# Kernel tuning notes

Measured on AMD Instinct MI355X. Metric: run time of the kernel, lower is better.

Reference implementation:

```python
import jax, jax.numpy as jnp
import numpy as np

B, H, L, DK, DV = 4, 16, 1024, 64, 64

def setup_inputs() -> dict:
    key = jax.random.key(0)
    k1, k2, k3, k4 = jax.random.split(key, 4)
    Q = jax.random.normal(k1, (B, H, L, DK), dtype=jnp.float32)
    K = jax.random.normal(k2, (B, H, L, DK), dtype=jnp.float32)
    V = jax.random.normal(k3, (B, H, L, DV), dtype=jnp.float32)
    attn_mask = jax.random.randint(k4, (B, H, L, L), 0, 2).astype(jnp.bool_)
    return {"Q": Q, "K": K, "V": V, "attn_mask": attn_mask}

def reference(Q, K, V, attn_mask):
    # NOTE: original torch code uses d_k = Q.size(1) == n_heads (a bug kept for fidelity)
    scale = 1.0 / jnp.sqrt(jnp.asarray(Q.shape[1], dtype=Q.dtype))
    scores = jnp.einsum('bhqd,bhkd->bhqk', Q, K) * scale
    scores = jnp.where(attn_mask, jnp.asarray(-1e9, dtype=scores.dtype), scores)
    attn = jax.nn.softmax(scores, axis=-1)
    context = jnp.einsum('bhqk,bhkv->bhqv', attn, V)
    return (context, attn)
```

## Files before the change

kernel.cpp:

```cpp
#include <hip/hip_runtime.h>
#include <hip/hip_bf16.h>

typedef _Float16 half8 __attribute__((ext_vector_type(8)));
typedef _Float16 half4 __attribute__((ext_vector_type(4)));
typedef _Float16 half2v __attribute__((ext_vector_type(2)));
typedef __fp16 fp16x2 __attribute__((ext_vector_type(2)));
typedef float f32x4 __attribute__((ext_vector_type(4)));

#define BH_ 64
#define L_ 1024
#define DK_ 64

__device__ __forceinline__ unsigned short f2h(float f) {
    _Float16 h = (_Float16)f;
    return __builtin_bit_cast(unsigned short, h);
}
__device__ __forceinline__ unsigned int pk2h(float a, float b) {
    fp16x2 h = __builtin_amdgcn_cvt_pkrtz(a, b);
    return __builtin_bit_cast(unsigned int, h);
}

__global__ void prep_k(const float* __restrict__ K, unsigned short* __restrict__ Kh) {
    int idx = blockIdx.x * 256 + threadIdx.x;
    float4 v = reinterpret_cast<const float4*>(K)[idx];
    ushort4 o;
    o.x = f2h(v.x); o.y = f2h(v.y); o.z = f2h(v.z); o.w = f2h(v.w);
    reinterpret_cast<ushort4*>(Kh)[idx] = o;
}

__global__ void prep_v(const float* __restrict__ V, unsigned short* __restrict__ Vt) {
    __shared__ float lds[64][65];
    int bh = blockIdx.x >> 4, kt = blockIdx.x & 15;
    int t = threadIdx.x;
    const float* Vb = V + ((size_t)bh * L_ + kt * 64) * DK_;
#pragma unroll
    for (int it = 0; it < 4; ++it) {
        int idx = it * 256 + t;
        int row = idx >> 4, c4 = idx & 15;
        float4 v = reinterpret_cast<const float4*>(Vb + (size_t)row * DK_)[c4];
        lds[row][c4 * 4 + 0] = v.x; lds[row][c4 * 4 + 1] = v.y;
        lds[row][c4 * 4 + 2] = v.z; lds[row][c4 * 4 + 3] = v.w;
    }
    __syncthreads();
    unsigned short* Vtb = Vt + (size_t)bh * 64 * L_ + kt * 64;
#pragma unroll
    for (int it = 0; it < 4; ++it) {
        int idx = it * 256 + t;
        int n = idx >> 4, c4 = idx & 15;
        ushort4 o;
        o.x = f2h(lds[c4 * 4 + 0][n]);
        o.y = f2h(lds[c4 * 4 + 1][n]);
        o.z = f2h(lds[c4 * 4 + 2][n]);
        o.w = f2h(lds[c4 * 4 + 3][n]);
        *reinterpret_cast<ushort4*>(Vtb + (size_t)n * L_ + c4 * 4) = o;
    }
}

__global__ __launch_bounds__(256, 4) void attn_main(
    const float* __restrict__ Q, const int* __restrict__ mask,
    const unsigned short* __restrict__ Kh, const unsigned short* __restrict__ Vt,
    float* __restrict__ ctx_out, float* __restrict__ attn_out)
{
    const int qt = blockIdx.x, bh = blockIdx.y;
    const int tid = threadIdx.x;
    const int w = tid >> 6;
    const int lane = tid & 63;
    const int lg = lane >> 4, lr = lane & 15;
    const int q0 = qt * 16;

    __shared__ unsigned char mnib[16][272];
    __shared__ float red[2][4][16];
    __shared__ union {
        unsigned short p[16][1024];
        float ctxbuf[4][16][68];
    } u;

    auto paddr = [&](int row, int col) -> unsigned short* {
        unsigned byte = (unsigned)row * 2048u +
                        (((unsigned)col * 2u) ^ (((unsigned)(row & 7)) << 4));
        return (unsigned short*)((char*)&u.p[0][0] + byte);
    };

#pragma unroll
    for (int rr = 0; rr < 4; ++rr) {
        const int row = w * 4 + rr;
        const int* mrow = mask + ((size_t)bh * L_ + q0 + row) * L_;
#pragma unroll
        for (int j = 0; j < 4; ++j) {
            int4 v = *reinterpret_cast<const int4*>(mrow + j * 256 + lane * 4);
            unsigned nib = unsigned(v.x != 0)
                         | (unsigned(v.y != 0) << 1)
                         | (unsigned(v.z != 0) << 2)
                         | (unsigned(v.w != 0) << 3);
            mnib[row][j * 64 + lane] = (unsigned char)nib;
        }
    }

    half8 qh[2];
    {
        const float* qp = Q + ((size_t)bh * L_ + q0 + lr) * DK_ + lg * 8;
#pragma unroll
        for (int f = 0; f < 2; ++f) {
            float4 a = *reinterpret_cast<const float4*>(qp + f * 32);
            float4 b = *reinterpret_cast<const float4*>(qp + f * 32 + 4);
            qh[f][0] = (_Float16)a.x; qh[f][1] = (_Float16)a.y;
            qh[f][2] = (_Float16)a.z; qh[f][3] = (_Float16)a.w;
            qh[f][4] = (_Float16)b.x; qh[f][5] = (_Float16)b.y;
            qh[f][6] = (_Float16)b.z; qh[f][7] = (_Float16)b.w;
        }
    }
    __syncthreads();

    const unsigned short* kp = Kh + ((size_t)bh * L_ + w * 256 + lr) * DK_ + lg * 8;
    const unsigned char* mn = &mnib[lr][w * 64];
    unsigned int sh[16][2];
    float mx = -INFINITY;

    half8 kc0 = *reinterpret_cast<const half8*>(kp);
    half8 kc1 = *reinterpret_cast<const half8*>(kp + 32);

#pragma unroll
    for (int tt = 0; tt < 16; ++tt) {
        half8 kn0 = kc0, kn1 = kc1;
        if (tt < 15) {
            kn0 = *reinterpret_cast<const half8*>(kp + (tt + 1) * 1024);
            kn1 = *reinterpret_cast<const half8*>(kp + (tt + 1) * 1024 + 32);
        }
        f32x4 acc = {0.f, 0.f, 0.f, 0.f};
        acc = __builtin_amdgcn_mfma_f32_16x16x32_f16(kc0, qh[0], acc, 0, 0, 0);
        acc = __builtin_amdgcn_mfma_f32_16x16x32_f16(kc1, qh[1], acc, 0, 0, 0);
        unsigned nv = *reinterpret_cast<const unsigned int*>(&mn[tt * 4]);
        unsigned nib = (nv >> (lg * 8)) & 0xFu;
        float s0 = (nib & 1u) ? -INFINITY : 0.25f * acc[0];
        float s1 = (nib & 2u) ? -INFINITY : 0.25f * acc[1];
        float s2 = (nib & 4u) ? -INFINITY : 0.25f * acc[2];
        float s3 = (nib & 8u) ? -INFINITY : 0.25f * acc[3];
        sh[tt][0] = pk2h(s0, s1);
        sh[tt][1] = pk2h(s2, s3);
        mx = fmaxf(mx, fmaxf(fmaxf(s0, s1), fmaxf(s2, s3)));
        kc0 = kn0; kc1 = kn1;
    }

    mx = fmaxf(mx, __shfl_xor(mx, 16));
    mx = fmaxf(mx, __shfl_xor(mx, 32));
    if (lane < 16) red[0][w][lr] = mx;
    __syncthreads();
    const float gm = fmaxf(fmaxf(red[0][0][lr], red[0][1][lr]),
                           fmaxf(red[0][2][lr], red[0][3][lr]));

    float lsum = 0.f;
#pragma unroll
    for (int tt = 0; tt < 16; ++tt) {
        half2v a = __builtin_bit_cast(half2v, sh[tt][0]);
        half2v b = __builtin_bit_cast(half2v, sh[tt][1]);
        float p0 = __expf((float)a[0] - gm);
        float p1 = __expf((float)a[1] - gm);
        float p2 = __expf((float)b[0] - gm);
        float p3 = __expf((float)b[1] - gm);
        lsum += (p0 + p1) + (p2 + p3);
        sh[tt][0] = pk2h(p0, p1);
        sh[tt][1] = pk2h(p2, p3);
    }
    lsum += __shfl_xor(lsum, 16);
    lsum += __shfl_xor(lsum, 32);
    if (lane < 16) red[1][w][lr] = lsum;

#pragma unroll
    for (int tt = 0; tt < 16; ++tt) {
        uint2 pr; pr.x = sh[tt][0]; pr.y = sh[tt][1];
        *reinterpret_cast<uint2*>(paddr(lr, w * 256 + tt * 16 + lg * 4)) = pr;
    }

    const unsigned short* vp = Vt + ((size_t)bh * 64 + lr) * L_ + w * 256 + lg * 8;
    f32x4 cacc[4] = {{0,0,0,0},{0,0,0,0},{0,0,0,0},{0,0,0,0}};
    half8 vb0 = *reinterpret_cast<const half8*>(vp);
    half8 vb1 = *reinterpret_cast<const half8*>(vp + 16384);
    half8 vb2 = *reinterpret_cast<const half8*>(vp + 32768);
    half8 vb3 = *reinterpret_cast<const half8*>(vp + 49152);

#pragma unroll
    for (int c = 0; c < 8; ++c) {
        half8 vn0 = vb0, vn1 = vb1, vn2 = vb2, vn3 = vb3;
        if (c < 7) {
            vn0 = *reinterpret_cast<const half8*>(vp + (c + 1) * 32);
            vn1 = *reinterpret_cast<const half8*>(vp + 16384 + (c + 1) * 32);
            vn2 = *reinterpret_cast<const half8*>(vp + 32768 + (c + 1) * 32);
            vn3 = *reinterpret_cast<const half8*>(vp + 49152 + (c + 1) * 32);
        }
        half8 pa = *reinterpret_cast<const half8*>(paddr(lr, w * 256 + c * 32 + lg * 8));
        cacc[0] = __builtin_amdgcn_mfma_f32_16x16x32_f16(pa, vb0, cacc[0], 0, 0, 0);
        cacc[1] = __builtin_amdgcn_mfma_f32_16x16x32_f16(pa, vb1, cacc[1], 0, 0, 0);
        cacc[2] = __builtin_amdgcn_mfma_f32_16x16x32_f16(pa, vb2, cacc[2], 0, 0, 0);
        cacc[3] = __builtin_amdgcn_mfma_f32_16x16x32_f16(pa, vb3, cacc[3], 0, 0, 0);
        vb0 = vn0; vb1 = vn1; vb2 = vn2; vb3 = vn3;
    }

    __syncthreads();

    half4 preg[4][4];
    float rqv[4];
#pragma unroll
    for (int rr = 0; rr < 4; ++rr) {
        const int q = w * 4 + rr;
        rqv[rr] = 1.0f / (red[1][0][q] + red[1][1][q] +
                          red[1][2][q] + red[1][3][q]);
#pragma unroll
        for (int i = 0; i < 4; ++i)
            preg[rr][i] = *reinterpret_cast<const half4*>(paddr(q, i * 256 + lane * 4));
    }

    __syncthreads();

#pragma unroll
    for (int nt = 0; nt < 4; ++nt)
#pragma unroll
        for (int r = 0; r < 4; ++r)
            u.ctxbuf[w][lg * 4 + r][nt * 16 + lr] = cacc[nt][r];
    __syncthreads();
    {
        int e = tid * 4;
        int q = e >> 6, n = e & 63;
        float gs = red[1][0][q] + red[1][1][q] + red[1][2][q] + red[1][3][q];
        float rq = 1.0f / gs;
        float4 a0 = *reinterpret_cast<float4*>(&u.ctxbuf[0][q][n]);
        float4 a1 = *reinterpret_cast<float4*>(&u.ctxbuf[1][q][n]);
        float4 a2 = *reinterpret_cast<float4*>(&u.ctxbuf[2][q][n]);
        float4 a3 = *reinterpret_cast<float4*>(&u.ctxbuf[3][q][n]);
        float4 o;
        o.x = (a0.x + a1.x + a2.x + a3.x) * rq;
        o.y = (a0.y + a1.y + a2.y + a3.y) * rq;
        o.z = (a0.z + a1.z + a2.z + a3.z) * rq;
        o.w = (a0.w + a1.w + a2.w + a3.w) * rq;
        *reinterpret_cast<float4*>(&ctx_out[((size_t)bh * L_ + q0 + q) * DK_ + n]) = o;
    }

#pragma unroll
    for (int rr = 0; rr < 4; ++rr) {
        const int q = w * 4 + rr;
        const float rq = rqv[rr];
        float* orow = attn_out + ((size_t)bh * L_ + q0 + q) * L_;
#pragma unroll
        for (int i = 0; i < 4; ++i) {
            half4 v = preg[rr][i];
            float4 o;
            o.x = (float)v[0] * rq; o.y = (float)v[1] * rq;
            o.z = (float)v[2] * rq; o.w = (float)v[3] * rq;
            *reinterpret_cast<float4*>(orow + i * 256 + lane * 4) = o;
        }
    }
}

extern "C" void kernel_launch(void* const* d_in, const int* in_sizes, int n_in,
                              void* d_out, int out_size, void* d_ws, size_t ws_size,
                              hipStream_t stream) {
    const float* Q = (const float*)d_in[0];
    const float* K = (const float*)d_in[1];
    const float* V = (const float*)d_in[2];
    const int* mask = (const int*)d_in[3];
    float* ctx_out = (float*)d_out;
    float* attn_out = ctx_out + (size_t)BH_ * L_ * DK_;

    unsigned short* Kh = (unsigned short*)d_ws;
    unsigned short* Vt = Kh + (size_t)BH_ * L_ * DK_;

    hipLaunchKernelGGL(prep_k, dim3(4096), dim3(256), 0, stream, K, Kh);
    hipLaunchKernelGGL(prep_v, dim3(1024), dim3(256), 0, stream, V, Vt);
    hipLaunchKernelGGL(attn_main, dim3(64, 64), dim3(256), 0, stream,
                       Q, mask, Kh, Vt, ctx_out, attn_out);
}
```

Baseline: 204.5 us.

## Load mask into registers late and merge K/V prep kernels

The main kernel no longer stages the mask into LDS as packed nibbles behind a barrier at kernel start. Instead each lane loads its own int4 mask chunks straight into registers, split around the row-max reduction, and zeroes masked probabilities in the exp phase. The row max is now taken over unmasked and masked scores alike, which is still correct by shift invariance unless a whole row is masked. The two prep kernels are merged into one launch. This adds about 64 VGPRs of live mask state under a 4-waves launch bound, which risks spilling or lower occupancy.

```diff
diff --git a/kernel.cpp b/kernel.cpp
--- a/kernel.cpp
+++ b/kernel.cpp
@@ -6,6 +6,7 @@
 typedef _Float16 half2v __attribute__((ext_vector_type(2)));
 typedef __fp16 fp16x2 __attribute__((ext_vector_type(2)));
 typedef float f32x4 __attribute__((ext_vector_type(4)));
+typedef int i32x4 __attribute__((ext_vector_type(4)));
 
 #define BH_ 64
 #define L_ 1024
@@ -20,17 +21,19 @@
     return __builtin_bit_cast(unsigned int, h);
 }
 
-__global__ void prep_k(const float* __restrict__ K, unsigned short* __restrict__ Kh) {
-    int idx = blockIdx.x * 256 + threadIdx.x;
-    float4 v = reinterpret_cast<const float4*>(K)[idx];
-    ushort4 o;
-    o.x = f2h(v.x); o.y = f2h(v.y); o.z = f2h(v.z); o.w = f2h(v.w);
-    reinterpret_cast<ushort4*>(Kh)[idx] = o;
-}
-
-__global__ void prep_v(const float* __restrict__ V, unsigned short* __restrict__ Vt) {
+__global__ void prep_kv(const float* __restrict__ K, const float* __restrict__ V,
+                        unsigned short* __restrict__ Kh, unsigned short* __restrict__ Vt) {
     __shared__ float lds[64][65];
-    int bh = blockIdx.x >> 4, kt = blockIdx.x & 15;
+    if (blockIdx.x < 4096) {
+        int idx = blockIdx.x * 256 + threadIdx.x;
+        float4 v = reinterpret_cast<const float4*>(K)[idx];
+        ushort4 o;
+        o.x = f2h(v.x); o.y = f2h(v.y); o.z = f2h(v.z); o.w = f2h(v.w);
+        reinterpret_cast<ushort4*>(Kh)[idx] = o;
+        return;
+    }
+    int b = blockIdx.x - 4096;
+    int bh = b >> 4, kt = b & 15;
     int t = threadIdx.x;
     const float* Vb = V + ((size_t)bh * L_ + kt * 64) * DK_;
 #pragma unroll
@@ -68,7 +71,6 @@
     const int lg = lane >> 4, lr = lane & 15;
     const int q0 = qt * 16;
 
-    __shared__ unsigned char mnib[16][272];
     __shared__ float red[2][4][16];
     __shared__ union {
         unsigned short p[16][1024];
@@ -80,21 +82,6 @@
                         (((unsigned)col * 2u) ^ (((unsigned)(row & 7)) << 4));
         return (unsigned short*)((char*)&u.p[0][0] + byte);
     };
-
-#pragma unroll
-    for (int rr = 0; rr < 4; ++rr) {
-        const int row = w * 4 + rr;
-        const int* mrow = mask + ((size_t)bh * L_ + q0 + row) * L_;
-#pragma unroll
-        for (int j = 0; j < 4; ++j) {
-            int4 v = *reinterpret_cast<const int4*>(mrow + j * 256 + lane * 4);
-            unsigned nib = unsigned(v.x != 0)
-                         | (unsigned(v.y != 0) << 1)
-                         | (unsigned(v.z != 0) << 2)
-                         | (unsigned(v.w != 0) << 3);
-            mnib[row][j * 64 + lane] = (unsigned char)nib;
-        }
-    }
 
     half8 qh[2];
     {
@@ -109,10 +96,11 @@
             qh[f][6] = (_Float16)b.z; qh[f][7] = (_Float16)b.w;
         }
     }
-    __syncthreads();
-
+
+    const size_t rowbase = ((size_t)bh * L_ + q0 + lr) * L_;
     const unsigned short* kp = Kh + ((size_t)bh * L_ + w * 256 + lr) * DK_ + lg * 8;
-    const unsigned char* mn = &mnib[lr][w * 64];
+    const int* mp = mask + rowbase + w * 256 + lg * 4;
+
     unsigned int sh[16][2];
     float mx = -INFINITY;
 
@@ -129,18 +117,21 @@
         f32x4 acc = {0.f, 0.f, 0.f, 0.f};
         acc = __builtin_amdgcn_mfma_f32_16x16x32_f16(kc0, qh[0], acc, 0, 0, 0);
         acc = __builtin_amdgcn_mfma_f32_16x16x32_f16(kc1, qh[1], acc, 0, 0, 0);
-        unsigned nv = *reinterpret_cast<const unsigned int*>(&mn[tt * 4]);
-        unsigned nib = (nv >> (lg * 8)) & 0xFu;
-        float s0 = (nib & 1u) ? -INFINITY : 0.25f * acc[0];
-        float s1 = (nib & 2u) ? -INFINITY : 0.25f * acc[1];
-        float s2 = (nib & 4u) ? -INFINITY : 0.25f * acc[2];
-        float s3 = (nib & 8u) ? -INFINITY : 0.25f * acc[3];
+        float s0 = 0.25f * acc[0];
+        float s1 = 0.25f * acc[1];
+        float s2 = 0.25f * acc[2];
+        float s3 = 0.25f * acc[3];
         sh[tt][0] = pk2h(s0, s1);
         sh[tt][1] = pk2h(s2, s3);
         mx = fmaxf(mx, fmaxf(fmaxf(s0, s1), fmaxf(s2, s3)));
         kc0 = kn0; kc1 = kn1;
     }
 
+    i32x4 mreg0[8];
+#pragma unroll
+    for (int tt = 0; tt < 8; ++tt)
+        mreg0[tt] = *reinterpret_cast<const i32x4*>(mp + tt * 16);
+
     mx = fmaxf(mx, __shfl_xor(mx, 16));
     mx = fmaxf(mx, __shfl_xor(mx, 32));
     if (lane < 16) red[0][w][lr] = mx;
@@ -148,15 +139,21 @@
     const float gm = fmaxf(fmaxf(red[0][0][lr], red[0][1][lr]),
                            fmaxf(red[0][2][lr], red[0][3][lr]));
 
+    i32x4 mreg1[8];
+#pragma unroll
+    for (int tt = 0; tt < 8; ++tt)
+        mreg1[tt] = *reinterpret_cast<const i32x4*>(mp + (tt + 8) * 16);
+
     float lsum = 0.f;
 #pragma unroll
     for (int tt = 0; tt < 16; ++tt) {
         half2v a = __builtin_bit_cast(half2v, sh[tt][0]);
         half2v b = __builtin_bit_cast(half2v, sh[tt][1]);
-        float p0 = __expf((float)a[0] - gm);
-        float p1 = __expf((float)a[1] - gm);
-        float p2 = __expf((float)b[0] - gm);
-        float p3 = __expf((float)b[1] - gm);
+        i32x4 m = (tt < 8) ? mreg0[tt] : mreg1[tt - 8];
+        float p0 = m[0] ? 0.f : __expf((float)a[0] - gm);
+        float p1 = m[1] ? 0.f : __expf((float)a[1] - gm);
+        float p2 = m[2] ? 0.f : __expf((float)b[0] - gm);
+        float p3 = m[3] ? 0.f : __expf((float)b[1] - gm);
         lsum += (p0 + p1) + (p2 + p3);
         sh[tt][0] = pk2h(p0, p1);
         sh[tt][1] = pk2h(p2, p3);
@@ -263,8 +260,7 @@
     unsigned short* Kh = (unsigned short*)d_ws;
     unsigned short* Vt = Kh + (size_t)BH_ * L_ * DK_;
 
-    hipLaunchKernelGGL(prep_k, dim3(4096), dim3(256), 0, stream, K, Kh);
-    hipLaunchKernelGGL(prep_v, dim3(1024), dim3(256), 0, stream, V, Vt);
+    hipLaunchKernelGGL(prep_kv, dim3(5120), dim3(256), 0, stream, K, V, Kh, Vt);
     hipLaunchKernelGGL(attn_main, dim3(64, 64), dim3(256), 0, stream,
                        Q, mask, Kh, Vt, ctx_out, attn_out);
 }
```

Measured after the change: 215.1 us. 1.05x slower.
